# Kernel tuning notes

Hardware: AMD Instinct MI355X
Metric: run time of the kernel (lower is better)

The kernel has to match this reference:

```python
import jax, jax.numpy as jnp
import numpy as np

ALPHA = 0.2  # leaky relu slope
NEG_INF = -9e15  # matches torch constant -9000000000000000.0


def setup_inputs() -> dict:
    key = jax.random.key(0)
    k1, k2, k3, k4, k5 = jax.random.split(key, 5)
    B, S, FIN, FOUT, H = 1, 4096, 128, 64, 8
    input_seq = jax.random.normal(k1, (B, S, FIN), dtype=jnp.float32)
    adj = jax.random.randint(k2, (B, S, S), 0, 2, dtype=jnp.int32)
    W = jax.random.normal(k3, (H, FIN, FOUT), dtype=jnp.float32) * 0.1
    a_1 = jax.random.normal(k4, (H, FOUT, 1), dtype=jnp.float32) * 0.1
    a_2 = jax.random.normal(k5, (H, FOUT, 1), dtype=jnp.float32) * 0.1
    return {"input_seq": input_seq, "adj": adj, "W": W, "a_1": a_1, "a_2": a_2}


def reference(input_seq, adj, W, a_1, a_2):
    B, S, _ = input_seq.shape
    H, _, FOUT = W.shape
    # h: [B, H, S, FOUT]
    h = jnp.einsum('bni,hio->bhno', input_seq, W)
    f1 = jnp.einsum('bhno,hoz->bhnz', h, a_1)[..., 0]  # [B,H,S]
    f2 = jnp.einsum('bhno,hoz->bhnz', h, a_2)[..., 0]  # [B,H,S]
    # e[b,h,i,j] = f1[i] + f2[j]
    e = jax.nn.leaky_relu(f1[:, :, :, None] + f2[:, :, None, :], ALPHA)
    mask = adj[:, None, :, :] > 0  # [B,1,S,S] broadcast over heads
    e = jnp.where(mask, e, NEG_INF)
    # NOTE: original softmax is over dim=2 (source-node axis), not -1
    attention = jax.nn.softmax(e, axis=2)
    # dropout is inference-mode no-op
    node_out = jnp.einsum('bhij,bhjo->bhio', attention, h)  # [B,H,S,FOUT]
    node_out = jnp.transpose(node_out, (0, 2, 1, 3)).reshape(B, S, H * FOUT)
    node_out = jax.nn.elu(node_out)
    return jnp.squeeze(node_out)
```

## Files before the change

kernel.cpp:

```cpp
#include <hip/hip_runtime.h>

#define S 4096
#define PS 4128
#define FIN 128
#define FOUT 64
#define H 8
#define ALPHA 0.2f

typedef __attribute__((ext_vector_type(2)))  _Float16 f16x2;
typedef __attribute__((ext_vector_type(8)))  _Float16 f16x8;
typedef __attribute__((ext_vector_type(16))) float    f32x16;

__device__ __forceinline__ unsigned short f2h(float x) {
    return __builtin_bit_cast(unsigned short, (_Float16)x);
}

__global__ __launch_bounds__(256) void k_proj(const float* __restrict__ X,
                                              const float* __restrict__ W,
                                              const float* __restrict__ a1,
                                              const float* __restrict__ a2,
                                              unsigned short* __restrict__ hT,
                                              float2* __restrict__ E1h,
                                              float2* __restrict__ E2p) {
    __shared__ float xs[64][36];
    __shared__ float Ws[32][68];
    const int h  = blockIdx.y;
    const int j0 = blockIdx.x * 64;
    const int t  = threadIdx.x;
    const int fg = t & 15, rg = t >> 4;
    const int jr = t >> 2, q = t & 3;
    const int kw = t >> 3, cw = t & 7;
    float acc[4][4] = {};
#pragma unroll
    for (int k0 = 0; k0 < FIN; k0 += 32) {
        *(float4*)&xs[jr][q * 8]      = *(const float4*)&X[(j0 + jr) * FIN + k0 + q * 8];
        *(float4*)&xs[jr][q * 8 + 4]  = *(const float4*)&X[(j0 + jr) * FIN + k0 + q * 8 + 4];
        *(float4*)&Ws[kw][cw * 8]     = *(const float4*)&W[(h * FIN + k0 + kw) * FOUT + cw * 8];
        *(float4*)&Ws[kw][cw * 8 + 4] = *(const float4*)&W[(h * FIN + k0 + kw) * FOUT + cw * 8 + 4];
        __syncthreads();
#pragma unroll
        for (int kc = 0; kc < 8; ++kc) {
            float4 xr[4], wr[4];
#pragma unroll
            for (int r = 0; r < 4; ++r) xr[r] = *(const float4*)&xs[4 * rg + r][kc * 4];
#pragma unroll
            for (int kk = 0; kk < 4; ++kk) wr[kk] = *(const float4*)&Ws[kc * 4 + kk][fg * 4];
#pragma unroll
            for (int r = 0; r < 4; ++r) {
                const float* xp = (const float*)&xr[r];
#pragma unroll
                for (int kk = 0; kk < 4; ++kk) {
                    const float xv = xp[kk];
                    acc[r][0] += xv * wr[kk].x;
                    acc[r][1] += xv * wr[kk].y;
                    acc[r][2] += xv * wr[kk].z;
                    acc[r][3] += xv * wr[kk].w;
                }
            }
        }
        __syncthreads();
    }
    const float4 a1v = *(const float4*)&a1[h * FOUT + fg * 4];
    const float4 a2v = *(const float4*)&a2[h * FOUT + fg * 4];
#pragma unroll
    for (int r = 0; r < 4; ++r) {
        float p1 = acc[r][0] * a1v.x + acc[r][1] * a1v.y + acc[r][2] * a1v.z + acc[r][3] * a1v.w;
        float p2 = acc[r][0] * a2v.x + acc[r][1] * a2v.y + acc[r][2] * a2v.z + acc[r][3] * a2v.w;
#pragma unroll
        for (int off = 1; off < 16; off <<= 1) {
            p1 += __shfl_xor(p1, off, 64);
            p2 += __shfl_xor(p2, off, 64);
        }
        if (fg == 0) {
            const int row = j0 + 4 * rg + r;
            E1h[(size_t)row * H + h] = make_float2(__expf(p1), __expf(ALPHA * p1));
            E2p[h * S + row]         = make_float2(__expf(p2), __expf(ALPHA * p2));
        }
    }
#pragma unroll
    for (int c = 0; c < 4; ++c) {
        ushort4 pk;
        pk.x = f2h(acc[0][c]);
        pk.y = f2h(acc[1][c]);
        pk.z = f2h(acc[2][c]);
        pk.w = f2h(acc[3][c]);
        *(ushort4*)&hT[(size_t)(h * FOUT + fg * 4 + c) * PS + j0 + 4 * rg] = pk;
    }
}

__global__ __launch_bounds__(256) void k_colsum(const int* __restrict__ adj,
                                                const float2* __restrict__ E1h,
                                                const float2* __restrict__ E2p,
                                                float* __restrict__ Dpart,
                                                unsigned int* __restrict__ bmT) {
    __shared__ float red[4][H][64];
    const int j0    = blockIdx.x * 64;
    const int ibase = blockIdx.y * 128;
    const int t  = threadIdx.x;
    const int jl = t & 63;
    const int wv = __builtin_amdgcn_readfirstlane(t >> 6);
    float2 e2v[H];
    float Dl[H];
#pragma unroll
    for (int hh = 0; hh < H; ++hh) { e2v[hh] = E2p[hh * S + j0 + jl]; Dl[hh] = 0.f; }
    const int rowbase = ibase + wv * 32;
    for (int s = 0; s < 32; s += 8) {
        int av[8];
#pragma unroll
        for (int u = 0; u < 8; ++u)
            av[u] = adj[(size_t)(rowbase + s + u) * S + j0 + jl];
#pragma unroll
        for (int u = 0; u < 8; ++u) {
            const int row = rowbase + s + u;
            const float2* __restrict__ e1r = E1h + (size_t)row * H;
            const unsigned long long blt = __ballot(av[u] != 0);
            if (jl == 0) {
                bmT[(j0 >> 5) * S + row]       = (unsigned int)blt;
                bmT[((j0 >> 5) + 1) * S + row] = (unsigned int)(blt >> 32);
            }
            const float bf = av[u] != 0 ? 1.f : 0.f;
#pragma unroll
            for (int hh = 0; hh < H; ++hh) {
                const float2 e1 = e1r[hh];
                Dl[hh] = fmaf(bf, fmaxf(e1.x * e2v[hh].x, e1.y * e2v[hh].y), Dl[hh]);
            }
        }
    }
#pragma unroll
    for (int hh = 0; hh < H; ++hh) red[wv][hh][jl] = Dl[hh];
    __syncthreads();
    if (wv == 0) {
#pragma unroll
        for (int hh = 0; hh < H; ++hh) {
            const float sum = red[0][hh][jl] + red[1][hh][jl] +
                              red[2][hh][jl] + red[3][hh][jl];
            Dpart[(blockIdx.y * H + hh) * S + j0 + jl] = sum;
        }
    }
}

__global__ __launch_bounds__(256) void k_finish(const float* __restrict__ Dpart,
                                                const float2* __restrict__ E2p,
                                                uint2* __restrict__ wE2h) {
    const int idx = blockIdx.x * 256 + threadIdx.x;
    const int hh = idx >> 11, pp = idx & 2047;
    const int j = 2 * pp;
    float sx = 0.f, sy = 0.f;
#pragma unroll
    for (int z = 0; z < 32; ++z) {
        const float2 d = *(const float2*)&Dpart[(z * H + hh) * S + j];
        sx += d.x; sy += d.y;
    }
    const float4 e2 = *(const float4*)&E2p[hh * S + j];
    const float wa = 1.0f / sx, wb = 1.0f / sy;
    f16x2 qx, qy;
    qx[0] = (_Float16)(e2.x * wa); qx[1] = (_Float16)(e2.z * wb);
    qy[0] = (_Float16)(e2.y * wa); qy[1] = (_Float16)(e2.w * wb);
    wE2h[idx] = make_uint2(__builtin_bit_cast(unsigned int, qx),
                           __builtin_bit_cast(unsigned int, qy));
}

__global__ __launch_bounds__(512, 4) void k_attn(const unsigned int* __restrict__ bmT,
                                                 const float2* __restrict__ E1h,
                                                 const uint2* __restrict__ wE2h,
                                                 const unsigned short* __restrict__ hT,
                                                 float* __restrict__ outp) {
    __shared__ __align__(16) char smem[40960];
    const int h  = blockIdx.y;
    const int i0 = blockIdx.x * 128;
    const int z  = blockIdx.z;
    const int t  = threadIdx.x;

    uint2* wE2s = (uint2*)(smem + 32768);
    ((uint4*)wE2s)[t] = ((const uint4*)(wE2h + h * (S / 2) + z * 1024))[t];

    const int lane = t & 63, wv = t >> 6;
    const int q  = wv >> 2;
    const int mw = wv & 3;
    const int am = lane & 31, kh = lane >> 5;
    const int i  = i0 + mw * 32 + am;
    const int jbase = z * 2048 + q * 1024;

    const float2 e1 = E1h[(size_t)i * H + h];
    f16x2 ea2, eb2;
    ea2[0] = ea2[1] = (_Float16)e1.x;
    eb2[0] = eb2[1] = (_Float16)e1.y;

    f32x16 acc0 = {0,0,0,0,0,0,0,0,0,0,0,0,0,0,0,0};
    f32x16 acc1 = {0,0,0,0,0,0,0,0,0,0,0,0,0,0,0,0};

    const int tq = t & 255;
    const int sf = tq >> 2;
    const int c0 = tq & 3;
    unsigned short* Bq = (unsigned short*)smem + q * 8192;
    const unsigned short* hstage = hT + (size_t)(h * FOUT + sf) * PS + jbase;

    const unsigned int* bmcol = bmT + (jbase >> 5) * S + i;
    const uint2* e2s = wE2s + q * 512 + kh * 4;
    const unsigned int sh = kh * 8;

    uint4 va = *(const uint4*)(hstage + c0 * 8);
    uint4 vb = *(const uint4*)(hstage + 32 + c0 * 8);
    unsigned int bw0 = bmcol[0];
    unsigned int bw1 = bmcol[S];
    __syncthreads();

    for (int jt = 0; jt < 16; ++jt) {
        unsigned short* Bc = Bq + (jt & 1) * 4096;
        *(uint4*)&Bc[sf * 64 + ((c0 ^ (sf & 7)) * 8)]       = va;
        *(uint4*)&Bc[sf * 64 + (((c0 + 4) ^ (sf & 7)) * 8)] = vb;
        const unsigned int m0 = bw0, m1 = bw1;
        __syncthreads();
        if (jt < 15) {
            va  = *(const uint4*)(hstage + (jt + 1) * 64 + c0 * 8);
            vb  = *(const uint4*)(hstage + (jt + 1) * 64 + 32 + c0 * 8);
            bw0 = bmcol[(2 * jt + 2) * S];
            bw1 = bmcol[(2 * jt + 3) * S];
        }
        unsigned int bys[4];
        bys[0] = (m0 >> sh) & 0xffu;
        bys[1] = (m0 >> (sh + 16)) & 0xffu;
        bys[2] = (m1 >> sh) & 0xffu;
        bys[3] = (m1 >> (sh + 16)) & 0xffu;
#pragma unroll
        for (int s = 0; s < 4; ++s) {
            const uint4 eA = *(const uint4*)(e2s + jt * 32 + s * 8);
            const uint4 eB = *(const uint4*)(e2s + jt * 32 + s * 8 + 2);
            const unsigned int by = bys[s];
            uint4 aw;
#define GAT_PAIR(pp, qxu, qyu, dst)                                               \
            {                                                                     \
                const f16x2 pa = ea2 * __builtin_bit_cast(f16x2, qxu);            \
                const f16x2 pb = eb2 * __builtin_bit_cast(f16x2, qyu);            \
                const f16x2 pm = __builtin_elementwise_max(pa, pb);               \
                const unsigned int b2 = (by >> (2 * pp)) & 3u;                    \
                const unsigned int vv = (b2 | (b2 << 15)) & 0x00010001u;          \
                const unsigned int mm = (vv << 14) - (vv << 10);    \
                dst = __builtin_bit_cast(unsigned int,                            \
                      pm * __builtin_bit_cast(f16x2, mm));                        \
            }
            GAT_PAIR(0, eA.x, eA.y, aw.x)
            GAT_PAIR(1, eA.z, eA.w, aw.y)
            GAT_PAIR(2, eB.x, eB.y, aw.z)
            GAT_PAIR(3, eB.z, eB.w, aw.w)
#undef GAT_PAIR
            const int chunk = s * 2 + kh;
            const f16x8 a  = __builtin_bit_cast(f16x8, aw);
            const f16x8 b0 = *(const f16x8*)&Bc[am * 64 + ((chunk ^ (am & 7)) * 8)];
            const f16x8 b1 = *(const f16x8*)&Bc[(am + 32) * 64 + ((chunk ^ ((am + 32) & 7)) * 8)];
            acc0 = __builtin_amdgcn_mfma_f32_32x32x16_f16(a, b0, acc0, 0, 0, 0);
            acc1 = __builtin_amdgcn_mfma_f32_32x32x16_f16(a, b1, acc1, 0, 0, 0);
        }
    }
    __syncthreads();

    float* r1 = (float*)smem;
    const int ro = (mw * 64 + lane) * 36;
    if (q == 1) {
#pragma unroll
        for (int r = 0; r < 16; ++r) { r1[ro + r] = acc0[r]; r1[ro + 16 + r] = acc1[r]; }
    }
    __syncthreads();
    if (q == 0) {
#pragma unroll
        for (int r = 0; r < 16; ++r) { acc0[r] += r1[ro + r]; acc1[r] += r1[ro + 16 + r]; }
        float* dst = outp + (size_t)z * (S * H * FOUT);
#pragma unroll
        for (int r = 0; r < 16; ++r) {
            const int il  = (r & 3) + 8 * (r >> 2) + 4 * kh;
            const int row = i0 + mw * 32 + il;
            dst[row * (H * FOUT) + h * FOUT + am]      = acc0[r];
            dst[row * (H * FOUT) + h * FOUT + 32 + am] = acc1[r];
        }
    }
}

__global__ __launch_bounds__(256) void k_elu(const float* __restrict__ outp,
                                             float* __restrict__ out) {
    const int idx = (blockIdx.x * 256 + threadIdx.x) * 4;
    const float4 p0 = *(const float4*)&outp[idx];
    const float4 p1 = *(const float4*)&outp[S * H * FOUT + idx];
    float4 v;
    v.x = p0.x + p1.x; v.y = p0.y + p1.y; v.z = p0.z + p1.z; v.w = p0.w + p1.w;
    v.x = v.x > 0.f ? v.x : __expf(v.x) - 1.f;
    v.y = v.y > 0.f ? v.y : __expf(v.y) - 1.f;
    v.z = v.z > 0.f ? v.z : __expf(v.z) - 1.f;
    v.w = v.w > 0.f ? v.w : __expf(v.w) - 1.f;
    *(float4*)&out[idx] = v;
}

extern "C" void kernel_launch(void* const* d_in, const int* in_sizes, int n_in,
                              void* d_out, int out_size, void* d_ws, size_t ws_size,
                              hipStream_t stream) {
    const float* X   = (const float*)d_in[0];
    const int*   adj = (const int*)d_in[1];
    const float* W   = (const float*)d_in[2];
    const float* a1  = (const float*)d_in[3];
    const float* a2  = (const float*)d_in[4];
    float* out = (float*)d_out;

    char* ws = (char*)d_ws;
    unsigned short* hT   = (unsigned short*)ws;
    float2*         E1h  = (float2*)(ws + 4325376);
    float2*         E2p  = (float2*)(ws + 4587520);
    float*          Dpart= (float*)(ws + 4849664);
    unsigned int*   bmT  = (unsigned int*)(ws + 9043968);
    uint2*          wE2h = (uint2*)(ws + 11141120);
    float*          outp = (float*)(ws + 11272192);

    k_proj  <<<dim3(S / 64, H),       256, 0, stream>>>(X, W, a1, a2, hT, E1h, E2p);
    k_colsum<<<dim3(S / 64, S / 128), 256, 0, stream>>>(adj, E1h, E2p, Dpart, bmT);
    k_finish<<<dim3(H * S / 512),     256, 0, stream>>>(Dpart, E2p, wE2h);
    k_attn  <<<dim3(S / 128, H, 2),   512, 0, stream>>>(bmT, E1h, wE2h, hT, outp);
    k_elu   <<<dim3(S * H * FOUT / 1024), 256, 0, stream>>>(outp, out);
}
```

Baseline: 174.1 us.

## Split attention K dimension across four smaller blocks instead of in-block halves

The attention kernel now uses 256-thread blocks, each covering one 1024-wide slice of source nodes, with four z-slices in the grid. Previously 512-thread blocks had two wave groups reduce through shared memory. This removes the in-block LDS reduction and its barriers, halves shared memory per block and doubles the block count to improve occupancy and load balance. The ELU kernel now sums four partial outputs instead of two, which adds global write and read traffic and needs more workspace for the partial buffers.

```diff
diff --git a/kernel.cpp b/kernel.cpp
--- a/kernel.cpp
+++ b/kernel.cpp
@@ -160,26 +160,24 @@
                            __builtin_bit_cast(unsigned int, qy));
 }
 
-__global__ __launch_bounds__(512, 4) void k_attn(const unsigned int* __restrict__ bmT,
+__global__ __launch_bounds__(256, 6) void k_attn(const unsigned int* __restrict__ bmT,
                                                  const float2* __restrict__ E1h,
                                                  const uint2* __restrict__ wE2h,
                                                  const unsigned short* __restrict__ hT,
                                                  float* __restrict__ outp) {
-    __shared__ __align__(16) char smem[40960];
+    __shared__ __align__(16) char smem[20480];
     const int h  = blockIdx.y;
     const int i0 = blockIdx.x * 128;
     const int z  = blockIdx.z;
     const int t  = threadIdx.x;
-
-    uint2* wE2s = (uint2*)(smem + 32768);
-    ((uint4*)wE2s)[t] = ((const uint4*)(wE2h + h * (S / 2) + z * 1024))[t];
-
-    const int lane = t & 63, wv = t >> 6;
-    const int q  = wv >> 2;
-    const int mw = wv & 3;
+    const int jbase = z * 1024;
+
+    uint2* wE2s = (uint2*)(smem + 16384);
+    ((uint4*)wE2s)[t] = ((const uint4*)(wE2h + h * (S / 2) + (jbase >> 1)))[t & 255];
+
+    const int lane = t & 63, mw = t >> 6;
     const int am = lane & 31, kh = lane >> 5;
     const int i  = i0 + mw * 32 + am;
-    const int jbase = z * 2048 + q * 1024;
 
     const float2 e1 = E1h[(size_t)i * H + h];
     f16x2 ea2, eb2;
@@ -189,14 +187,13 @@
     f32x16 acc0 = {0,0,0,0,0,0,0,0,0,0,0,0,0,0,0,0};
     f32x16 acc1 = {0,0,0,0,0,0,0,0,0,0,0,0,0,0,0,0};
 
-    const int tq = t & 255;
-    const int sf = tq >> 2;
-    const int c0 = tq & 3;
-    unsigned short* Bq = (unsigned short*)smem + q * 8192;
+    const int sf = t >> 2;
+    const int c0 = t & 3;
+    unsigned short* Bq = (unsigned short*)smem;
     const unsigned short* hstage = hT + (size_t)(h * FOUT + sf) * PS + jbase;
 
     const unsigned int* bmcol = bmT + (jbase >> 5) * S + i;
-    const uint2* e2s = wE2s + q * 512 + kh * 4;
+    const uint2* e2s = wE2s + kh * 4;
     const unsigned int sh = kh * 8;
 
     uint4 va = *(const uint4*)(hstage + c0 * 8);
@@ -252,36 +249,26 @@
             acc1 = __builtin_amdgcn_mfma_f32_32x32x16_f16(a, b1, acc1, 0, 0, 0);
         }
     }
-    __syncthreads();
-
-    float* r1 = (float*)smem;
-    const int ro = (mw * 64 + lane) * 36;
-    if (q == 1) {
-#pragma unroll
-        for (int r = 0; r < 16; ++r) { r1[ro + r] = acc0[r]; r1[ro + 16 + r] = acc1[r]; }
-    }
-    __syncthreads();
-    if (q == 0) {
-#pragma unroll
-        for (int r = 0; r < 16; ++r) { acc0[r] += r1[ro + r]; acc1[r] += r1[ro + 16 + r]; }
-        float* dst = outp + (size_t)z * (S * H * FOUT);
-#pragma unroll
-        for (int r = 0; r < 16; ++r) {
-            const int il  = (r & 3) + 8 * (r >> 2) + 4 * kh;
-            const int row = i0 + mw * 32 + il;
-            dst[row * (H * FOUT) + h * FOUT + am]      = acc0[r];
-            dst[row * (H * FOUT) + h * FOUT + 32 + am] = acc1[r];
-        }
+
+    float* dst = outp + (size_t)z * (S * H * FOUT);
+#pragma unroll
+    for (int r = 0; r < 16; ++r) {
+        const int il  = (r & 3) + 8 * (r >> 2) + 4 * kh;
+        const int row = i0 + mw * 32 + il;
+        dst[row * (H * FOUT) + h * FOUT + am]      = acc0[r];
+        dst[row * (H * FOUT) + h * FOUT + 32 + am] = acc1[r];
     }
 }
 
 __global__ __launch_bounds__(256) void k_elu(const float* __restrict__ outp,
                                              float* __restrict__ out) {
     const int idx = (blockIdx.x * 256 + threadIdx.x) * 4;
-    const float4 p0 = *(const float4*)&outp[idx];
-    const float4 p1 = *(const float4*)&outp[S * H * FOUT + idx];
-    float4 v;
-    v.x = p0.x + p1.x; v.y = p0.y + p1.y; v.z = p0.z + p1.z; v.w = p0.w + p1.w;
+    float4 v = *(const float4*)&outp[idx];
+#pragma unroll
+    for (int z = 1; z < 4; ++z) {
+        const float4 p = *(const float4*)&outp[(size_t)z * (S * H * FOUT) + idx];
+        v.x += p.x; v.y += p.y; v.z += p.z; v.w += p.w;
+    }
     v.x = v.x > 0.f ? v.x : __expf(v.x) - 1.f;
     v.y = v.y > 0.f ? v.y : __expf(v.y) - 1.f;
     v.z = v.z > 0.f ? v.z : __expf(v.z) - 1.f;
@@ -311,6 +298,6 @@
     k_proj  <<<dim3(S / 64, H),       256, 0, stream>>>(X, W, a1, a2, hT, E1h, E2p);
     k_colsum<<<dim3(S / 64, S / 128), 256, 0, stream>>>(adj, E1h, E2p, Dpart, bmT);
     k_finish<<<dim3(H * S / 512),     256, 0, stream>>>(Dpart, E2p, wE2h);
-    k_attn  <<<dim3(S / 128, H, 2),   512, 0, stream>>>(bmT, E1h, wE2h, hT, outp);
+    k_attn  <<<dim3(S / 128, H, 4),   256, 0, stream>>>(bmT, E1h, wE2h, hT, outp);
     k_elu   <<<dim3(S * H * FOUT / 1024), 256, 0, stream>>>(outp, out);
 }
```

Result: slower. 178.3 us (+2.4%).
